# Optimization experiments

Measured on AMD Instinct MI355X. Metric: run time of the kernel, lower is better.

Reference implementation:

```python
import jax, jax.numpy as jnp
import numpy as np

B, T, C, H = 64, 256, 384, 6
HS = C // H  # 64


def _ln(x, w, b, eps=1e-5):
    m = jnp.mean(x, axis=-1, keepdims=True)
    v = jnp.mean((x - m) ** 2, axis=-1, keepdims=True)
    return (x - m) / jnp.sqrt(v + eps) * w + b


def setup_inputs() -> dict:
    key = jax.random.key(0)
    ks = jax.random.split(key, 18)
    sc = 0.02
    return {
        "x": jax.random.normal(ks[0], (B, T, C), jnp.float32),
        "ln1_w": jnp.ones((C,), jnp.float32),
        "ln1_b": jnp.zeros((C,), jnp.float32),
        # per-head Q/K/V linears stacked over the head axis: [H, C, HS]
        "Wq": jax.random.normal(ks[1], (H, C, HS), jnp.float32) * sc,
        "bq": jnp.zeros((H, HS), jnp.float32),
        "Wk": jax.random.normal(ks[2], (H, C, HS), jnp.float32) * sc,
        "bk": jnp.zeros((H, HS), jnp.float32),
        "Wv": jax.random.normal(ks[3], (H, C, HS), jnp.float32) * sc,
        "bv": jnp.zeros((H, HS), jnp.float32),
        "Wproj": jax.random.normal(ks[4], (C, C), jnp.float32) * sc,
        "bproj": jnp.zeros((C,), jnp.float32),
        "ln2_w": jnp.ones((C,), jnp.float32),
        "ln2_b": jnp.zeros((C,), jnp.float32),
        "W1": jax.random.normal(ks[5], (C, 4 * C), jnp.float32) * sc,
        "b1": jnp.zeros((4 * C,), jnp.float32),
        "W2": jax.random.normal(ks[6], (4 * C, C), jnp.float32) * sc,
        "b2": jnp.zeros((C,), jnp.float32),
    }


def reference(x, ln1_w, ln1_b, Wq, bq, Wk, bk, Wv, bv, Wproj, bproj,
              ln2_w, ln2_b, W1, b1, W2, b2):
    # --- pre-norm causal MHA (dropout = identity in eval) ---
    h = _ln(x, ln1_w, ln1_b)
    Q = jnp.einsum('btc,hcd->bhtd', h, Wq) + bq[None, :, None, :]
    K = jnp.einsum('btc,hcd->bhtd', h, Wk) + bk[None, :, None, :]
    V = jnp.einsum('btc,hcd->bhtd', h, Wv) + bv[None, :, None, :]
    scores = jnp.einsum('bhtd,bhsd->bhts', Q, K) * (HS ** -0.5)
    mask = jnp.tril(jnp.ones((x.shape[1], x.shape[1]), bool))
    scores = jnp.where(mask, scores, -jnp.inf)
    wei = jax.nn.softmax(scores, axis=-1)
    o = jnp.einsum('bhts,bhsd->bhtd', wei, V)
    # concat heads (same order as torch.cat over head list)
    o = o.transpose(0, 2, 1, 3).reshape(x.shape[0], x.shape[1], C)
    x1 = x + o @ Wproj + bproj
    # --- pre-norm FFN with exact (erf) GELU, matching torch default ---
    h2 = _ln(x1, ln2_w, ln2_b)
    f = jax.nn.gelu(h2 @ W1 + b1, approximate=False) @ W2 + b2
    return x1 + f
```

## Files before the change

kernel.cpp:

```cpp
#include <hip/hip_runtime.h>
#include <math.h>

constexpr int Bsz  = 64;
constexpr int Tseq = 256;
constexpr int Cdim = 384;
constexpr int Hh   = 6;
constexpr int HSd  = 64;
constexpr int Mrows = Bsz * Tseq;
constexpr int Cffn  = 4 * Cdim;
constexpr int Nqkv  = 3 * Cdim;

typedef __attribute__((ext_vector_type(8))) short short8;
typedef __attribute__((ext_vector_type(4))) float f32x4;

__device__ __forceinline__ ushort f2bf(float x) {
  union { float f; uint u; } a; a.f = x;
  uint r = a.u + 0x7fffu + ((a.u >> 16) & 1u);
  return (ushort)(r >> 16);
}
__device__ __forceinline__ float bf2f(ushort u) {
  union { uint u; float f; } a; a.u = ((uint)u) << 16;
  return a.f;
}
__device__ __forceinline__ uint pk_bf16(float lo, float hi) {
  uint r;
  asm("v_cvt_pk_bf16_f32 %0, %1, %2" : "=v"(r) : "v"(lo), "v"(hi));
  return r;
}

__device__ __forceinline__ float gelu_fast(float x) {
  float t = x * x;
  float u = x * fmaf(0.044715f, t, 1.0f);
  float e = fminf(1.5957691216f * u, 80.f);
  float z = __expf(e);
  return x * (z / (1.0f + z));
}

__global__ __launch_bounds__(256) void prep_kernel(
    const float* __restrict__ Wq, const float* __restrict__ Wk,
    const float* __restrict__ Wv, const float* __restrict__ Wproj,
    const float* __restrict__ W1, const float* __restrict__ W2,
    const float* __restrict__ bq, const float* __restrict__ bk,
    const float* __restrict__ bv,
    ushort* __restrict__ WqkvT, ushort* __restrict__ WprojT,
    ushort* __restrict__ W1T, ushort* __restrict__ W2T,
    float* __restrict__ bqkv) {
  const int bid = blockIdx.x;
  if (bid >= 1728) {
    int i = (bid - 1728) * 256 + threadIdx.x;
    if (i < Nqkv)
      bqkv[i] = (i < 384) ? bq[i] : (i < 768) ? bk[i - 384] : bv[i - 768];
    return;
  }
  const int tx = threadIdx.x & 31, ty = threadIdx.x >> 5;
  const float* src; ushort* dst; int R, S, r0, s0, perm = 0;
  if (bid < 432) {
    int which = bid / 144, rem = bid % 144;
    const float* W = (which == 0) ? Wq : (which == 1) ? Wk : Wv;
    int bz = rem / 24, t = rem % 24;
    R = 384; S = 64;
    src = W + (size_t)bz * R * S;
    dst = WqkvT + (size_t)which * 384 * 384 + (size_t)bz * R * S;
    r0 = (t >> 1) * 32; s0 = (t & 1) * 32;
  } else if (bid < 576) {
    int rem = bid - 432; R = 384; S = 384; src = Wproj; dst = WprojT;
    r0 = (rem / 12) * 32; s0 = (rem % 12) * 32; perm = 1;
  } else if (bid < 1152) {
    int rem = bid - 576; R = 384; S = 1536; src = W1; dst = W1T;
    r0 = (rem / 48) * 32; s0 = (rem % 48) * 32;
  } else {
    int rem = bid - 1152; R = 1536; S = 384; src = W2; dst = W2T;
    r0 = (rem / 12) * 32; s0 = (rem % 12) * 32; perm = 1;
  }
  __shared__ float t[32][33];
#pragma unroll
  for (int i = 0; i < 32; i += 8)
    t[ty + i][tx] = src[(size_t)(r0 + ty + i) * S + s0 + tx];
  __syncthreads();
  const int kk = r0 + tx;
  int kp = kk;
  if (perm) kp = (kk & ~63) | (((kk & 15) << 2) | ((kk >> 4) & 3));
#pragma unroll
  for (int i = 0; i < 32; i += 8)
    dst[(size_t)(s0 + ty + i) * R + kp] = f2bf(t[tx][ty + i]);
}

template <typename T>
__global__ __launch_bounds__(256) void ln_kernel(
    const T* __restrict__ x, const float* __restrict__ w,
    const float* __restrict__ b, ushort* __restrict__ out, int nrows) {
  int row  = blockIdx.x * 4 + (threadIdx.x >> 6);
  int lane = threadIdx.x & 63;
  if (row >= nrows) return;
  const T* xr = x + (size_t)row * Cdim;
  float v[6];
  float s = 0.f;
#pragma unroll
  for (int i = 0; i < 6; ++i) {
    if constexpr (sizeof(T) == 2) v[i] = bf2f(xr[lane + 64 * i]);
    else                          v[i] = xr[lane + 64 * i];
    s += v[i];
  }
#pragma unroll
  for (int off = 32; off > 0; off >>= 1) s += __shfl_xor(s, off, 64);
  float mean = s * (1.f / Cdim);
  float sq = 0.f;
#pragma unroll
  for (int i = 0; i < 6; ++i) { float d = v[i] - mean; sq += d * d; }
#pragma unroll
  for (int off = 32; off > 0; off >>= 1) sq += __shfl_xor(sq, off, 64);
  float rstd = rsqrtf(sq * (1.f / Cdim) + 1e-5f);
  ushort* orow = out + (size_t)row * Cdim;
#pragma unroll
  for (int i = 0; i < 6; ++i) {
    int c = lane + 64 * i;
    orow[c] = f2bf((v[i] - mean) * rstd * w[c] + b[c]);
  }
}

template <int EPI, int BN>
__global__ __launch_bounds__(256) void mfma_gemm(
    const ushort* __restrict__ A, const ushort* __restrict__ Bt,
    const float* __restrict__ bias, const void* __restrict__ res,
    void* __restrict__ Cout, void* __restrict__ C2, void* __restrict__ C3,
    int M, int N, int K) {
  constexpr int WC = BN / 2;
  constexpr int JN = WC / 16;
  constexpr int NB = BN / 32;
  __shared__ ushort Als[2 * 128 * 64];
  __shared__ ushort Bls[2 * BN * 64];
  const int tid = threadIdx.x;

  const int lid = blockIdx.y * gridDim.x + blockIdx.x;
  const int xcd = lid & 7, idx = lid >> 3;
  const int by = xcd * 16 + (idx & 15);
  const int bx = idx >> 4;
  const int m0 = by * 128, n0 = bx * BN;

  const int lane = tid & 63;
  const int w    = tid >> 6;
  const int wr   = (w >> 1) * 64;
  const int wc   = (w & 1) * WC;
  const int lm   = lane & 15;
  const int g    = lane >> 4;
  const int rq   = g * 4;

  const int wub = (tid & ~63) * 8;

  f32x4 acc[4][JN] = {};

  auto stage = [&](int k0, int bf) {
    ushort* Ab = Als + bf * (128 * 64);
    ushort* Bb = Bls + bf * (BN * 64);
#pragma unroll
    for (int q = 0; q < 4; ++q) {
      const int ci = tid + q * 256;
      const int row = ci >> 3;
      const int kc = ((ci & 7) ^ (row & 7)) * 8;
      const ushort* gA = A + (size_t)(m0 + row) * K + k0 + kc;
      __builtin_amdgcn_global_load_lds(
          (const __attribute__((address_space(1))) uint*)gA,
          (__attribute__((address_space(3))) uint*)(Ab + wub + q * 2048),
          16, 0, 0);
    }
#pragma unroll
    for (int q = 0; q < NB; ++q) {
      const int ci = tid + q * 256;
      const int row = ci >> 3;
      const int kc = ((ci & 7) ^ (row & 7)) * 8;
      const ushort* gB = Bt + (size_t)(n0 + row) * K + k0 + kc;
      __builtin_amdgcn_global_load_lds(
          (const __attribute__((address_space(1))) uint*)gB,
          (__attribute__((address_space(3))) uint*)(Bb + wub + q * 2048),
          16, 0, 0);
    }
  };

  const int nt = K >> 6;
  stage(0, 0);

  for (int t = 0; t < nt; ++t) {
    const int cur = t & 1;
    if (t + 1 < nt) {
      stage((t + 1) * 64, cur ^ 1);
      if constexpr (NB == 4)
        asm volatile("s_waitcnt vmcnt(8)" ::: "memory");
      else
        asm volatile("s_waitcnt vmcnt(6)" ::: "memory");
    } else {
      asm volatile("s_waitcnt vmcnt(0)" ::: "memory");
    }
    __builtin_amdgcn_sched_barrier(0);
    __builtin_amdgcn_s_barrier();
    __builtin_amdgcn_sched_barrier(0);

    const ushort* Ab = Als + cur * (128 * 64);
    const ushort* Bb = Bls + cur * (BN * 64);
#pragma unroll
    for (int half = 0; half < 2; ++half) {
      const int sl = ((half << 2) | g) ^ (lm & 7);
      short8 af[4], bfr[JN];
#pragma unroll
      for (int i = 0; i < 4; ++i)
        af[i] = *(const short8*)&Ab[(wr + i * 16 + lm) * 64 + sl * 8];
#pragma unroll
      for (int j = 0; j < JN; ++j)
        bfr[j] = *(const short8*)&Bb[(wc + j * 16 + lm) * 64 + sl * 8];
      __builtin_amdgcn_s_setprio(1);
#pragma unroll
      for (int i = 0; i < 4; ++i)
#pragma unroll
        for (int j = 0; j < JN; ++j)
          acc[i][j] = __builtin_amdgcn_mfma_f32_16x16x32_bf16(af[i], bfr[j],
                                                              acc[i][j], 0, 0, 0);
      __builtin_amdgcn_s_setprio(0);
    }

    asm volatile("s_waitcnt lgkmcnt(0)" ::: "memory");
    __builtin_amdgcn_sched_barrier(0);
    __builtin_amdgcn_s_barrier();
    __builtin_amdgcn_sched_barrier(0);
  }

  float bb[JN];
#pragma unroll
  for (int j = 0; j < JN; ++j) bb[j] = bias[n0 + wc + j * 16 + lm];

#pragma unroll
  for (int i = 0; i < 4; ++i) {
#pragma unroll
    for (int r = 0; r < 4; ++r) {
      const int row = m0 + wr + i * 16 + rq + r;
      if constexpr (EPI == 1) {
        const float* resrow = (const float*)res + (size_t)row * N + n0 + wc;
        ushort* crow = (ushort*)Cout + (size_t)row * N + n0 + wc;
#pragma unroll
        for (int j = 0; j < JN; ++j) {
          float rv = __builtin_nontemporal_load(resrow + j * 16 + lm);
          crow[j * 16 + lm] = f2bf(acc[i][j][r] + bb[j] + rv);
        }
      } else if constexpr (EPI == 4) {
        const ushort* resrow = (const ushort*)res + (size_t)row * N + n0 + wc;
        float* crow = (float*)Cout + (size_t)row * N + n0 + wc;
#pragma unroll
        for (int j = 0; j < JN; ++j)
          crow[j * 16 + lm] = acc[i][j][r] + bb[j] + bf2f(resrow[j * 16 + lm]);
      } else if constexpr (EPI == 3) {
        ushort* crow = (ushort*)Cout + (size_t)row * N + n0 + wc + lm * 4;
        uint d0 = pk_bf16(acc[i][0][r] + bb[0], acc[i][1][r] + bb[1]);
        uint d1 = pk_bf16(acc[i][2][r] + bb[2], acc[i][3][r] + bb[3]);
        uint2 pkv; pkv.x = d0; pkv.y = d1;
        *(uint2*)crow = pkv;
      } else {
        ushort* crow = (ushort*)Cout + (size_t)row * N + n0 + wc + lm * 4;
        float g0 = gelu_fast(acc[i][0][r] + bb[0]);
        float g1 = gelu_fast(acc[i][1][r] + bb[1]);
        float g2 = gelu_fast(acc[i][2][r] + bb[2]);
        float g3 = gelu_fast(acc[i][3][r] + bb[3]);
        uint d0 = pk_bf16(g0, g1);
        uint d1 = pk_bf16(g2, g3);
        uint2 pkv; pkv.x = d0; pkv.y = d1;
        *(uint2*)crow = pkv;
      }
    }
  }
}

__global__ __launch_bounds__(256) void attn_kernel(
    const ushort* __restrict__ QKV, ushort* __restrict__ Oc) {
  __shared__ ushort Ks[64 * 72];
  __shared__ ushort Vt[64 * 72];
  __shared__ ushort Pl[4][16 * 72];
  const int bh = blockIdx.x, qt = blockIdx.y;
  const int b = bh / Hh, h = bh % Hh;
  const int tid = threadIdx.x;
  const int w = tid >> 6, lane = tid & 63;
  const int g = lane >> 4, n16 = lane & 15;

  const ushort* qrow =
      QKV + (size_t)(b * Tseq + qt * 64 + w * 16 + n16) * Nqkv + h * HSd;
  short8 qf0 = *(const short8*)(qrow + g * 8);
  short8 qf1 = *(const short8*)(qrow + 32 + g * 8);

  f32x4 oacc[4] = {};
  float m_r[4], l_r[4];
#pragma unroll
  for (int r = 0; r < 4; ++r) { m_r[r] = -1e30f; l_r[r] = 0.f; }

  const int t0 = qt * 64 + w * 16 + g * 4;

  const ushort* Ksrc = QKV + (size_t)b * Tseq * Nqkv + Cdim + h * HSd;
  const ushort* Vsrc = QKV + (size_t)b * Tseq * Nqkv + 2 * Cdim + h * HSd;

  for (int st = 0; st <= qt; ++st) {
    __syncthreads();
    for (int c = tid; c < 512; c += 256) {
      int kr = c >> 3, kc = (c & 7) * 8;
      *(uint4*)&Ks[kr * 72 + kc] =
          *(const uint4*)&Ksrc[(size_t)(st * 64 + kr) * Nqkv + kc];
      int vr = c & 63, vc = (c >> 6) * 8;
      uint4 vv = *(const uint4*)&Vsrc[(size_t)(st * 64 + vr) * Nqkv + vc];
      const ushort* pv = (const ushort*)&vv;
#pragma unroll
      for (int i = 0; i < 8; ++i) Vt[(vc + i) * 72 + vr] = pv[i];
    }
    __syncthreads();

    f32x4 s[4];
#pragma unroll
    for (int ct = 0; ct < 4; ++ct) {
      short8 kf0 = *(const short8*)&Ks[(ct * 16 + n16) * 72 + g * 8];
      short8 kf1 = *(const short8*)&Ks[(ct * 16 + n16) * 72 + 32 + g * 8];
      f32x4 z = {};
      z = __builtin_amdgcn_mfma_f32_16x16x32_bf16(qf0, kf0, z, 0, 0, 0);
      z = __builtin_amdgcn_mfma_f32_16x16x32_bf16(qf1, kf1, z, 0, 0, 0);
      s[ct] = z;
    }

#pragma unroll
    for (int ct = 0; ct < 4; ++ct) {
      const int s_col = st * 64 + ct * 16 + n16;
#pragma unroll
      for (int r = 0; r < 4; ++r) {
        float v = s[ct][r] * 0.125f;
        s[ct][r] = (s_col > t0 + r) ? -1e30f : v;
      }
    }

#pragma unroll
    for (int r = 0; r < 4; ++r) {
      float m = fmaxf(fmaxf(s[0][r], s[1][r]), fmaxf(s[2][r], s[3][r]));
      m = fmaxf(m, __shfl_xor(m, 1, 64));
      m = fmaxf(m, __shfl_xor(m, 2, 64));
      m = fmaxf(m, __shfl_xor(m, 4, 64));
      m = fmaxf(m, __shfl_xor(m, 8, 64));
      float mnew = fmaxf(m_r[r], m);
      float alpha = __expf(m_r[r] - mnew);
      m_r[r] = mnew;
      float ssum = 0.f;
#pragma unroll
      for (int ct = 0; ct < 4; ++ct) {
        float p = __expf(s[ct][r] - mnew);
        s[ct][r] = p;
        ssum += p;
      }
      ssum += __shfl_xor(ssum, 1, 64);
      ssum += __shfl_xor(ssum, 2, 64);
      ssum += __shfl_xor(ssum, 4, 64);
      ssum += __shfl_xor(ssum, 8, 64);
      l_r[r] = l_r[r] * alpha + ssum;
#pragma unroll
      for (int j = 0; j < 4; ++j) oacc[j][r] *= alpha;
    }

    ushort* pw = &Pl[w][0];
#pragma unroll
    for (int ct = 0; ct < 4; ++ct)
#pragma unroll
      for (int r = 0; r < 4; ++r)
        pw[(g * 4 + r) * 72 + ct * 16 + n16] = f2bf(s[ct][r]);

    short8 pf0 = *(const short8*)&pw[n16 * 72 + g * 8];
    short8 pf1 = *(const short8*)&pw[n16 * 72 + 32 + g * 8];
#pragma unroll
    for (int j = 0; j < 4; ++j) {
      short8 vf0 = *(const short8*)&Vt[(j * 16 + n16) * 72 + g * 8];
      short8 vf1 = *(const short8*)&Vt[(j * 16 + n16) * 72 + 32 + g * 8];
      oacc[j] = __builtin_amdgcn_mfma_f32_16x16x32_bf16(pf0, vf0, oacc[j], 0, 0, 0);
      oacc[j] = __builtin_amdgcn_mfma_f32_16x16x32_bf16(pf1, vf1, oacc[j], 0, 0, 0);
    }
  }

  float inv[4];
#pragma unroll
  for (int r = 0; r < 4; ++r) inv[r] = 1.f / l_r[r];
  ushort* orow = Oc + ((size_t)(b * Tseq + qt * 64 + w * 16)) * Cdim + h * HSd;
#pragma unroll
  for (int j = 0; j < 4; ++j)
#pragma unroll
    for (int r = 0; r < 4; ++r)
      orow[(size_t)(g * 4 + r) * Cdim + j * 16 + n16] = f2bf(oacc[j][r] * inv[r]);
}

extern "C" void kernel_launch(void* const* d_in, const int* in_sizes, int n_in,
                              void* d_out, int out_size, void* d_ws, size_t ws_size,
                              hipStream_t stream) {
  const float* x      = (const float*)d_in[0];
  const float* ln1_w  = (const float*)d_in[1];
  const float* ln1_b  = (const float*)d_in[2];
  const float* Wq     = (const float*)d_in[3];
  const float* bq     = (const float*)d_in[4];
  const float* Wk     = (const float*)d_in[5];
  const float* bk     = (const float*)d_in[6];
  const float* Wv     = (const float*)d_in[7];
  const float* bv     = (const float*)d_in[8];
  const float* Wproj  = (const float*)d_in[9];
  const float* bproj  = (const float*)d_in[10];
  const float* ln2_w  = (const float*)d_in[11];
  const float* ln2_b  = (const float*)d_in[12];
  const float* W1     = (const float*)d_in[13];
  const float* b1     = (const float*)d_in[14];
  const float* W2     = (const float*)d_in[15];
  const float* b2     = (const float*)d_in[16];
  float* out = (float*)d_out;

  char* p = (char*)d_ws;
  ushort* h     = (ushort*)p;  p += (size_t)Mrows * Cdim * 2;
  ushort* QKV   = (ushort*)p;  p += (size_t)Mrows * Nqkv * 2;
  ushort* Oc    = (ushort*)p;  p += (size_t)Mrows * Cdim * 2;
  ushort* g     = (ushort*)p;  p += (size_t)Mrows * Cffn * 2;
  ushort* WqkvT = (ushort*)p;  p += (size_t)Nqkv * Cdim * 2;
  ushort* WprojT= (ushort*)p;  p += (size_t)Cdim * Cdim * 2;
  ushort* W1T   = (ushort*)p;  p += (size_t)Cffn * Cdim * 2;
  ushort* W2T   = (ushort*)p;  p += (size_t)Cdim * Cffn * 2;
  float*  bqkv  = (float*)p;   p += (size_t)Nqkv * 4;
  ushort* h2 = h;
  ushort* x1 = QKV;

  dim3 blk(256);

  prep_kernel<<<dim3(1733), blk, 0, stream>>>(Wq, Wk, Wv, Wproj, W1, W2,
                                              bq, bk, bv,
                                              WqkvT, WprojT, W1T, W2T, bqkv);

  ln_kernel<float><<<dim3(Mrows / 4), blk, 0, stream>>>(x, ln1_w, ln1_b, h, Mrows);

  mfma_gemm<3, 128><<<dim3(Nqkv / 128, Mrows / 128), blk, 0, stream>>>(
      h, WqkvT, bqkv, nullptr, QKV, nullptr, nullptr, Mrows, Nqkv, Cdim);

  attn_kernel<<<dim3(Bsz * Hh, 4), blk, 0, stream>>>(QKV, Oc);

  mfma_gemm<1, 64><<<dim3(Cdim / 64, Mrows / 128), blk, 0, stream>>>(
      Oc, WprojT, bproj, x, x1, nullptr, nullptr, Mrows, Cdim, Cdim);

  ln_kernel<ushort><<<dim3(Mrows / 4), blk, 0, stream>>>(x1, ln2_w, ln2_b, h2, Mrows);

  mfma_gemm<2, 128><<<dim3(Cffn / 128, Mrows / 128), blk, 0, stream>>>(
      h2, W1T, b1, nullptr, g, nullptr, nullptr, Mrows, Cffn, Cdim);

  mfma_gemm<4, 64><<<dim3(Cdim / 64, Mrows / 128), blk, 0, stream>>>(
      g, W2T, b2, x1, out, nullptr, nullptr, Mrows, Cdim, Cffn);
}
```

Before: 243.5 us.

## Fold LayerNorm2 affine into W1 and apply row stats in GEMM epilogue

Folds the ln2 weight into the W1 transpose and precomputes column sums of the scaled W1 along with an adjusted bias. The FFN1 GEMM then reads x1 directly and applies per-row mean and rstd in its epilogue. A small stats kernel that writes one float2 per row replaces the full LN2 kernel that wrote a normalized bf16 tensor. This removes one full-tensor write and read, but the mean subtraction now happens after the bf16 GEMM, which can cost precision through cancellation. The new column-sum blocks in prep are serial loops over 384 rows, which adds prep latency.

```diff
diff --git a/kernel.cpp b/kernel.cpp
--- a/kernel.cpp
+++ b/kernel.cpp
@@ -42,10 +42,25 @@
     const float* __restrict__ W1, const float* __restrict__ W2,
     const float* __restrict__ bq, const float* __restrict__ bk,
     const float* __restrict__ bv,
+    const float* __restrict__ ln2_w, const float* __restrict__ ln2_b,
+    const float* __restrict__ b1,
     ushort* __restrict__ WqkvT, ushort* __restrict__ WprojT,
     ushort* __restrict__ W1T, ushort* __restrict__ W2T,
-    float* __restrict__ bqkv) {
+    float* __restrict__ bqkv, float* __restrict__ sCol,
+    float* __restrict__ c2b) {
   const int bid = blockIdx.x;
+  if (bid >= 1733) {
+    const int n = (bid - 1733) * 256 + threadIdx.x;
+    float s1 = 0.f, s2 = 0.f;
+    for (int r = 0; r < Cdim; ++r) {
+      float v = W1[(size_t)r * Cffn + n];
+      s1 = fmaf(ln2_w[r], v, s1);
+      s2 = fmaf(ln2_b[r], v, s2);
+    }
+    sCol[n] = s1;
+    c2b[n] = s2 + b1[n];
+    return;
+  }
   if (bid >= 1728) {
     int i = (bid - 1728) * 256 + threadIdx.x;
     if (i < Nqkv)
@@ -54,6 +69,7 @@
   }
   const int tx = threadIdx.x & 31, ty = threadIdx.x >> 5;
   const float* src; ushort* dst; int R, S, r0, s0, perm = 0;
+  bool w1s = false;
   if (bid < 432) {
     int which = bid / 144, rem = bid % 144;
     const float* W = (which == 0) ? Wq : (which == 1) ? Wk : Wv;
@@ -67,7 +83,7 @@
     r0 = (rem / 12) * 32; s0 = (rem % 12) * 32; perm = 1;
   } else if (bid < 1152) {
     int rem = bid - 576; R = 384; S = 1536; src = W1; dst = W1T;
-    r0 = (rem / 48) * 32; s0 = (rem % 48) * 32;
+    r0 = (rem / 48) * 32; s0 = (rem % 48) * 32; w1s = true;
   } else {
     int rem = bid - 1152; R = 1536; S = 384; src = W2; dst = W2T;
     r0 = (rem / 12) * 32; s0 = (rem % 12) * 32; perm = 1;
@@ -80,9 +96,10 @@
   const int kk = r0 + tx;
   int kp = kk;
   if (perm) kp = (kk & ~63) | (((kk & 15) << 2) | ((kk >> 4) & 3));
+  const float sc = w1s ? ln2_w[kk] : 1.f;
 #pragma unroll
   for (int i = 0; i < 32; i += 8)
-    dst[(size_t)(s0 + ty + i) * R + kp] = f2bf(t[tx][ty + i]);
+    dst[(size_t)(s0 + ty + i) * R + kp] = f2bf(t[tx][ty + i] * sc);
 }
 
 template <typename T>
@@ -116,6 +133,28 @@
     int c = lane + 64 * i;
     orow[c] = f2bf((v[i] - mean) * rstd * w[c] + b[c]);
   }
+}
+
+__global__ __launch_bounds__(256) void stats_kernel(
+    const ushort* __restrict__ x, float2* __restrict__ st, int nrows) {
+  int row  = blockIdx.x * 4 + (threadIdx.x >> 6);
+  int lane = threadIdx.x & 63;
+  if (row >= nrows) return;
+  const ushort* xr = x + (size_t)row * Cdim;
+  float v[6];
+  float s = 0.f;
+#pragma unroll
+  for (int i = 0; i < 6; ++i) { v[i] = bf2f(xr[lane + 64 * i]); s += v[i]; }
+#pragma unroll
+  for (int off = 32; off > 0; off >>= 1) s += __shfl_xor(s, off, 64);
+  float mean = s * (1.f / Cdim);
+  float sq = 0.f;
+#pragma unroll
+  for (int i = 0; i < 6; ++i) { float d = v[i] - mean; sq += d * d; }
+#pragma unroll
+  for (int off = 32; off > 0; off >>= 1) sq += __shfl_xor(sq, off, 64);
+  float rstd = rsqrtf(sq * (1.f / Cdim) + 1e-5f);
+  if (lane == 0) st[row] = make_float2(rstd, rstd * mean);
 }
 
 template <int EPI, int BN>
@@ -225,6 +264,12 @@
   float bb[JN];
 #pragma unroll
   for (int j = 0; j < JN; ++j) bb[j] = bias[n0 + wc + j * 16 + lm];
+  float sj[JN] = {};
+  if constexpr (EPI == 5) {
+#pragma unroll
+    for (int j = 0; j < JN; ++j)
+      sj[j] = ((const float*)C2)[n0 + wc + j * 16 + lm];
+  }
 
 #pragma unroll
   for (int i = 0; i < 4; ++i) {
@@ -252,13 +297,14 @@
         uint2 pkv; pkv.x = d0; pkv.y = d1;
         *(uint2*)crow = pkv;
       } else {
+        const float2 st = ((const float2*)res)[row];
         ushort* crow = (ushort*)Cout + (size_t)row * N + n0 + wc + lm * 4;
-        float g0 = gelu_fast(acc[i][0][r] + bb[0]);
-        float g1 = gelu_fast(acc[i][1][r] + bb[1]);
-        float g2 = gelu_fast(acc[i][2][r] + bb[2]);
-        float g3 = gelu_fast(acc[i][3][r] + bb[3]);
-        uint d0 = pk_bf16(g0, g1);
-        uint d1 = pk_bf16(g2, g3);
+        float v0 = fmaf(st.x, acc[i][0][r], fmaf(-st.y, sj[0], bb[0]));
+        float v1 = fmaf(st.x, acc[i][1][r], fmaf(-st.y, sj[1], bb[1]));
+        float v2 = fmaf(st.x, acc[i][2][r], fmaf(-st.y, sj[2], bb[2]));
+        float v3 = fmaf(st.x, acc[i][3][r], fmaf(-st.y, sj[3], bb[3]));
+        uint d0 = pk_bf16(gelu_fast(v0), gelu_fast(v1));
+        uint d1 = pk_bf16(gelu_fast(v2), gelu_fast(v3));
         uint2 pkv; pkv.x = d0; pkv.y = d1;
         *(uint2*)crow = pkv;
       }
@@ -414,14 +460,17 @@
   ushort* W1T   = (ushort*)p;  p += (size_t)Cffn * Cdim * 2;
   ushort* W2T   = (ushort*)p;  p += (size_t)Cdim * Cffn * 2;
   float*  bqkv  = (float*)p;   p += (size_t)Nqkv * 4;
-  ushort* h2 = h;
+  float*  sCol  = (float*)p;   p += (size_t)Cffn * 4;
+  float*  c2b   = (float*)p;   p += (size_t)Cffn * 4;
+  float2* stats = (float2*)p;  p += (size_t)Mrows * sizeof(float2);
   ushort* x1 = QKV;
 
   dim3 blk(256);
 
-  prep_kernel<<<dim3(1733), blk, 0, stream>>>(Wq, Wk, Wv, Wproj, W1, W2,
-                                              bq, bk, bv,
-                                              WqkvT, WprojT, W1T, W2T, bqkv);
+  prep_kernel<<<dim3(1739), blk, 0, stream>>>(Wq, Wk, Wv, Wproj, W1, W2,
+                                              bq, bk, bv, ln2_w, ln2_b, b1,
+                                              WqkvT, WprojT, W1T, W2T,
+                                              bqkv, sCol, c2b);
 
   ln_kernel<float><<<dim3(Mrows / 4), blk, 0, stream>>>(x, ln1_w, ln1_b, h, Mrows);
 
@@ -433,10 +482,10 @@
   mfma_gemm<1, 64><<<dim3(Cdim / 64, Mrows / 128), blk, 0, stream>>>(
       Oc, WprojT, bproj, x, x1, nullptr, nullptr, Mrows, Cdim, Cdim);
 
-  ln_kernel<ushort><<<dim3(Mrows / 4), blk, 0, stream>>>(x1, ln2_w, ln2_b, h2, Mrows);
-
-  mfma_gemm<2, 128><<<dim3(Cffn / 128, Mrows / 128), blk, 0, stream>>>(
-      h2, W1T, b1, nullptr, g, nullptr, nullptr, Mrows, Cffn, Cdim);
+  stats_kernel<<<dim3(Mrows / 4), blk, 0, stream>>>(x1, stats, Mrows);
+
+  mfma_gemm<5, 128><<<dim3(Cffn / 128, Mrows / 128), blk, 0, stream>>>(
+      x1, W1T, c2b, stats, g, sCol, nullptr, Mrows, Cffn, Cdim);
 
   mfma_gemm<4, 64><<<dim3(Cdim / 64, Mrows / 128), blk, 0, stream>>>(
       g, W2T, b2, x1, out, nullptr, nullptr, Mrows, Cdim, Cffn);
```

Result: slower. 262.9 us (+8.0%).
